# Performance work log

Measured on AMD Instinct MI355X. Metric: run time of the kernel, lower is better.

The kernel has to match this reference:

```python
import jax, jax.numpy as jnp
import numpy as np

B = 8192
W = 48            # target-net width
P = 4849          # flat param size of target MLP(1->48->48->48->1)
HW = 96           # hypernet width = 2*W
STEPS = 20
LR = 0.1
B1, B2, EPS = 0.9, 0.999, 1e-8


def setup_inputs() -> dict:
    key = jax.random.key(0)
    ks = jax.random.split(key, 6)
    x = jax.random.normal(ks[0], (B, 1), dtype=jnp.float32)
    c = jax.random.normal(ks[1], (B, 1), dtype=jnp.float32)
    # hypernet params (Linear(2,96) -> relu -> Linear(96,4849)), He-ish scaling
    hw1 = jax.random.normal(ks[2], (HW, 2), dtype=jnp.float32) / jnp.sqrt(2.0)
    hb1 = jax.random.normal(ks[3], (HW,), dtype=jnp.float32) * 0.1
    hw2 = jax.random.normal(ks[4], (P, HW), dtype=jnp.float32) / jnp.sqrt(float(HW))
    hb2 = jax.random.normal(ks[5], (P,), dtype=jnp.float32) * 0.1
    return {"x": x, "c": c, "hw1": hw1, "hb1": hb1, "hw2": hw2, "hb2": hb2}


def _target_apply(p, y):
    # unflatten per tree_flatten order: (w,b) per Linear layer of MLP(1,48,48,48,1)
    w0 = p[0:48].reshape(W, 1);      b0 = p[48:96]
    w1 = p[96:2400].reshape(W, W);   b1 = p[2400:2448]
    w2 = p[2448:4752].reshape(W, W); b2 = p[4752:4800]
    w3 = p[4800:4848].reshape(1, W); b3 = p[4848:4849]
    h = jax.nn.swish(w0 @ y + b0)
    h = jax.nn.swish(w1 @ h + b1)
    h = jax.nn.swish(w2 @ h + b2)
    return jnp.squeeze(w3 @ h + b3)


def _taylor_energy_y(energy_fn, y_target, y_anchor):
    # 2nd-order Taylor expansion via nested JVPs (order_y == 2)
    tangent = y_target - y_anchor

    def grad_energy(y):
        return jax.jvp(energy_fn, (y,), (tangent,))[1]

    e0, term1 = jax.jvp(energy_fn, (y_anchor,), (tangent,))
    _, term2 = jax.jvp(grad_energy, (y_anchor,), (tangent,))
    return e0 + term1 + 0.5 * term2


def _energy(y, p, y_anchor):
    return _taylor_energy_y(lambda yi: _target_apply(p, yi), y, y_anchor)


_grad_fn = jax.vmap(jax.grad(_energy), in_axes=(0, 0, 0))  # grad wrt y only


def reference(x, c, hw1, hb1, hw2, hb2):
    hyper_in = jnp.concatenate([x, c], axis=1)                 # (B, 2)
    h = jax.nn.relu(hyper_in @ hw1.T + hb1)                    # (B, 96)
    flat_params = h @ hw2.T + hb2                              # (B, P)

    y0 = jnp.zeros((x.shape[0], 1), dtype=x.dtype)             # y_mean = 0.0
    m0 = jnp.zeros_like(y0)
    v0 = jnp.zeros_like(y0)

    def step(carry, _):
        y, m, v, t = carry
        g = _grad_fn(y, flat_params, y)  # key=None -> anchor y0 = y_curr
        t = t + 1
        m = B1 * m + (1.0 - B1) * g
        v = B2 * v + (1.0 - B2) * g * g
        mh = m / (1.0 - jnp.power(B1, t))
        vh = v / (1.0 - jnp.power(B2, t))
        y = y - LR * mh / (jnp.sqrt(vh) + EPS)
        return (y, m, v, t), None

    (y_final, _, _, _), _ = jax.lax.scan(
        step, (y0, m0, v0, jnp.asarray(0, jnp.int32)), None, length=STEPS)
    return y_final
```

## Files before the change

kernel.cpp:

```cpp
#include <hip/hip_runtime.h>
#include <cstdint>
#include <cstddef>

#define NB    8192
#define NP    4849
#define NW    48
#define NCH   38
#define GY    64

typedef __attribute__((ext_vector_type(8))) _Float16 f16x8;
typedef __attribute__((ext_vector_type(4))) float f32x4;
typedef __attribute__((ext_vector_type(2))) float f32x2;

__device__ __forceinline__ const float* pptr(const float* Pp, int i, int rp) {
  return Pp + ((size_t)(rp >> 7) * NB + i) * 128 + (rp & 127);
}

__device__ __forceinline__ int invperm(int rp) {
  if (rp >= 96 && rp < 2400) {
    int t = rp - 96; int kb = t / 192; int rem = t - kb * 192;
    return 96 + (rem >> 2) * 48 + (kb * 4 + (rem & 3));
  }
  if (rp >= 2448 && rp < 4752) {
    int t = rp - 2448; int kb = t / 192; int rem = t - kb * 192;
    return 2448 + (rem >> 2) * 48 + (kb * 4 + (rem & 3));
  }
  return rp;
}

__global__ __launch_bounds__(256, 2) void hyper_gemm(
    const float* __restrict__ x, const float* __restrict__ c,
    const float* __restrict__ hw1, const float* __restrict__ hb1,
    const float* __restrict__ hw2, const float* __restrict__ hb2,
    float* __restrict__ Pp)
{
  const int t    = threadIdx.x;
  const int lane = t & 63;
  const int wv   = t >> 6;
  const int m16  = lane & 15;
  const int q    = lane >> 4;
  const int rp0  = blockIdx.x * 128;

  const float* wr[2];
  float bias[2];
  #pragma unroll
  for (int nt = 0; nt < 2; ++nt) {
    int rp = rp0 + wv * 32 + nt * 16 + m16;
    int r  = (rp < NP) ? invperm(rp) : 0;
    wr[nt]   = hw2 + (size_t)r * 96;
    bias[nt] = (rp < NP) ? hb2[r] : 0.f;
  }

  f16x8 bh[3][2], bl[3][2];
  #pragma unroll
  for (int ch = 0; ch < 3; ++ch) {
    const int k0 = ch * 32 + q * 8;
    #pragma unroll
    for (int nt = 0; nt < 2; ++nt) {
      float4 f0 = *(const float4*)(wr[nt] + k0);
      float4 f1 = *(const float4*)(wr[nt] + k0 + 4);
      float fv[8] = {f0.x,f0.y,f0.z,f0.w,f1.x,f1.y,f1.z,f1.w};
      #pragma unroll
      for (int e = 0; e < 8; ++e) {
        _Float16 hi = (_Float16)fv[e];
        float r = fv[e] - (float)hi;
        bh[ch][nt][e] = hi;
        bl[ch][nt][e] = (_Float16)r;
      }
    }
  }

  float* cbase = Pp + (size_t)blockIdx.x * NB * 128;

  for (int mtile = blockIdx.y; mtile < 128; mtile += GY) {
    const int i0 = mtile * 64;

    float xv[4], cv[4];
    #pragma unroll
    for (int mt = 0; mt < 4; ++mt) {
      int i = i0 + mt * 16 + m16;
      xv[mt] = x[i]; cv[mt] = c[i];
    }

    f32x4 acc[4][2];
    #pragma unroll
    for (int mt = 0; mt < 4; ++mt)
      #pragma unroll
      for (int nt = 0; nt < 2; ++nt)
        acc[mt][nt] = (f32x4){0.f, 0.f, 0.f, 0.f};

    #pragma unroll
    for (int ch = 0; ch < 3; ++ch) {
      const int k0 = ch * 32 + q * 8;

      float4 A0 = *(const float4*)(hw1 + 2 * k0);
      float4 A1 = *(const float4*)(hw1 + 2 * k0 + 4);
      float4 A2 = *(const float4*)(hw1 + 2 * k0 + 8);
      float4 A3 = *(const float4*)(hw1 + 2 * k0 + 12);
      float4 B0 = *(const float4*)(hb1 + k0);
      float4 B1 = *(const float4*)(hb1 + k0 + 4);
      float w0k[8] = {A0.x,A0.z,A1.x,A1.z,A2.x,A2.z,A3.x,A3.z};
      float w1k[8] = {A0.y,A0.w,A1.y,A1.w,A2.y,A2.w,A3.y,A3.w};
      float bk[8]  = {B0.x,B0.y,B0.z,B0.w,B1.x,B1.y,B1.z,B1.w};

      f16x8 ah[4], al[4];
      #pragma unroll
      for (int mt = 0; mt < 4; ++mt) {
        #pragma unroll
        for (int j = 0; j < 8; ++j) {
          float h = fmaf(xv[mt], w0k[j], fmaf(cv[mt], w1k[j], bk[j]));
          h = h > 0.f ? h : 0.f;
          _Float16 hi = (_Float16)h;
          float r = h - (float)hi;
          ah[mt][j] = hi;
          al[mt][j] = (_Float16)r;
        }
      }

      #pragma unroll
      for (int mt = 0; mt < 4; ++mt)
        #pragma unroll
        for (int nt = 0; nt < 2; ++nt) {
          acc[mt][nt] = __builtin_amdgcn_mfma_f32_16x16x32_f16(al[mt], bl[ch][nt], acc[mt][nt], 0, 0, 0);
          acc[mt][nt] = __builtin_amdgcn_mfma_f32_16x16x32_f16(ah[mt], bl[ch][nt], acc[mt][nt], 0, 0, 0);
          acc[mt][nt] = __builtin_amdgcn_mfma_f32_16x16x32_f16(al[mt], bh[ch][nt], acc[mt][nt], 0, 0, 0);
          acc[mt][nt] = __builtin_amdgcn_mfma_f32_16x16x32_f16(ah[mt], bh[ch][nt], acc[mt][nt], 0, 0, 0);
        }
    }

    #pragma unroll
    for (int nt = 0; nt < 2; ++nt) {
      int off = wv * 32 + nt * 16 + m16;
      if (rp0 + off < NP) {
        #pragma unroll
        for (int mt = 0; mt < 4; ++mt)
          #pragma unroll
          for (int r = 0; r < 4; ++r) {
            int i = i0 + mt * 16 + q * 4 + r;
            cbase[(size_t)i * 128 + off] = acc[mt][nt][r] + bias[nt];
          }
      }
    }
  }
}


#define DPP_ADD(x, ctrl, rmask)                                               \
  (x) += __int_as_float(__builtin_amdgcn_update_dpp(                          \
      0, __float_as_int(x), (ctrl), (rmask), 0xf, false))

__global__ __launch_bounds__(64, 2) void adam_inner(
    const float* __restrict__ Pp, float* __restrict__ out)
{
  __shared__ __align__(16) float hd[2][96];

  const int lane = threadIdx.x;
  const int i    = blockIdx.x;
  const bool act = lane < NW;

  float* buf0 = &hd[0][0];
  float* buf1 = &hd[1][0];

  float w0  = act ? *pptr(Pp, i, lane)        : 0.f;
  float b0  = act ? *pptr(Pp, i, 48 + lane)   : 0.f;
  float b1v = act ? *pptr(Pp, i, 2400 + lane) : 0.f;
  float b2v = act ? *pptr(Pp, i, 4752 + lane) : 0.f;
  float w3  = act ? *pptr(Pp, i, 4800 + lane) : 0.f;

  f32x2 w1p[24], w2p[24];
  #pragma unroll
  for (int kb = 0; kb < 12; ++kb) {
    float4 q1 = *(const float4*)pptr(Pp, i, 96 + kb * 192 + lane * 4);
    w1p[2 * kb]     = (f32x2){q1.x, q1.y};
    w1p[2 * kb + 1] = (f32x2){q1.z, q1.w};
    float4 q2 = *(const float4*)pptr(Pp, i, 2448 + kb * 192 + lane * 4);
    w2p[2 * kb]     = (f32x2){q2.x, q2.y};
    w2p[2 * kb + 1] = (f32x2){q2.z, q2.w};
  }

  float y = 0.f, m = 0.f, v = 0.f;
  float b1t = 1.f, b2t = 1.f;

  #pragma unroll 1
  for (int t = 0; t < 20; ++t) {
    float z  = fmaf(w0, y, b0);
    float s  = __builtin_amdgcn_rcpf(1.f + __expf(-z));
    float h  = z * s;
    float dh = fmaf(z * s, 1.f - s, s) * w0;
    if (act) { buf0[lane] = h; buf0[48 + lane] = dh; }

    float4 ph[12], pd[12];
    #pragma unroll
    for (int kk = 0; kk < 12; ++kk) {
      ph[kk] = *(const float4*)(buf0 + 4 * kk);
      pd[kk] = *(const float4*)(buf0 + 48 + 4 * kk);
    }
    {
      f32x2 zz[4] = {(f32x2){b1v, 0.f}, (f32x2){0.f, 0.f},
                     (f32x2){0.f, 0.f}, (f32x2){0.f, 0.f}};
      f32x2 dd[4] = {(f32x2){0.f, 0.f}, (f32x2){0.f, 0.f},
                     (f32x2){0.f, 0.f}, (f32x2){0.f, 0.f}};
      #pragma unroll
      for (int kk = 0; kk < 12; ++kk) {
        int c0 = (2 * kk) & 3, c1 = (2 * kk + 1) & 3;
        zz[c0] = __builtin_elementwise_fma(w1p[2 * kk],     (f32x2){ph[kk].x, ph[kk].y}, zz[c0]);
        zz[c1] = __builtin_elementwise_fma(w1p[2 * kk + 1], (f32x2){ph[kk].z, ph[kk].w}, zz[c1]);
        dd[c0] = __builtin_elementwise_fma(w1p[2 * kk],     (f32x2){pd[kk].x, pd[kk].y}, dd[c0]);
        dd[c1] = __builtin_elementwise_fma(w1p[2 * kk + 1], (f32x2){pd[kk].z, pd[kk].w}, dd[c1]);
      }
      f32x2 zs = (zz[0] + zz[1]) + (zz[2] + zz[3]);
      f32x2 ds = (dd[0] + dd[1]) + (dd[2] + dd[3]);
      float z1  = zs.x + zs.y;
      float dz1 = ds.x + ds.y;

      s  = __builtin_amdgcn_rcpf(1.f + __expf(-z1));
      h  = z1 * s;
      dh = fmaf(h, 1.f - s, s) * dz1;
    }
    if (act) { buf1[lane] = h; buf1[48 + lane] = dh; }

    #pragma unroll
    for (int kk = 0; kk < 12; ++kk) {
      ph[kk] = *(const float4*)(buf1 + 4 * kk);
      pd[kk] = *(const float4*)(buf1 + 48 + 4 * kk);
    }
    {
      f32x2 zz[4] = {(f32x2){b2v, 0.f}, (f32x2){0.f, 0.f},
                     (f32x2){0.f, 0.f}, (f32x2){0.f, 0.f}};
      f32x2 dd[4] = {(f32x2){0.f, 0.f}, (f32x2){0.f, 0.f},
                     (f32x2){0.f, 0.f}, (f32x2){0.f, 0.f}};
      #pragma unroll
      for (int kk = 0; kk < 12; ++kk) {
        int c0 = (2 * kk) & 3, c1 = (2 * kk + 1) & 3;
        zz[c0] = __builtin_elementwise_fma(w2p[2 * kk],     (f32x2){ph[kk].x, ph[kk].y}, zz[c0]);
        zz[c1] = __builtin_elementwise_fma(w2p[2 * kk + 1], (f32x2){ph[kk].z, ph[kk].w}, zz[c1]);
        dd[c0] = __builtin_elementwise_fma(w2p[2 * kk],     (f32x2){pd[kk].x, pd[kk].y}, dd[c0]);
        dd[c1] = __builtin_elementwise_fma(w2p[2 * kk + 1], (f32x2){pd[kk].z, pd[kk].w}, dd[c1]);
      }
      f32x2 zs = (zz[0] + zz[1]) + (zz[2] + zz[3]);
      f32x2 ds = (dd[0] + dd[1]) + (dd[2] + dd[3]);
      float z2  = zs.x + zs.y;
      float dz2 = ds.x + ds.y;

      s  = __builtin_amdgcn_rcpf(1.f + __expf(-z2));
      dh = fmaf(z2 * s, 1.f - s, s) * dz2;
    }

    float r = act ? w3 * dh : 0.f;
    DPP_ADD(r, 0x111, 0xf);
    DPP_ADD(r, 0x112, 0xf);
    DPP_ADD(r, 0x114, 0xf);
    DPP_ADD(r, 0x118, 0xf);
    DPP_ADD(r, 0x142, 0xa);
    DPP_ADD(r, 0x143, 0xc);
    float g = __int_as_float(__builtin_amdgcn_readlane(__float_as_int(r), 63));

    m = fmaf(0.9f,   m, 0.1f   * g);
    v = fmaf(0.999f, v, 0.001f * g * g);
    b1t *= 0.9f; b2t *= 0.999f;
    float mh  = m * __builtin_amdgcn_rcpf(1.f - b1t);
    float vh  = v * __builtin_amdgcn_rcpf(1.f - b2t);
    float den = __builtin_amdgcn_sqrtf(vh) + 1e-8f;
    y -= 0.1f * mh * __builtin_amdgcn_rcpf(den);
  }

  if (lane == 0) out[i] = y;
}

extern "C" void kernel_launch(void* const* d_in, const int* in_sizes, int n_in,
                              void* d_out, int out_size, void* d_ws, size_t ws_size,
                              hipStream_t stream) {
  const float* x   = (const float*)d_in[0];
  const float* c   = (const float*)d_in[1];
  const float* hw1 = (const float*)d_in[2];
  const float* hb1 = (const float*)d_in[3];
  const float* hw2 = (const float*)d_in[4];
  const float* hb2 = (const float*)d_in[5];
  float* Pp  = (float*)d_ws;
  float* out = (float*)d_out;

  dim3 gridB(NCH, GY);
  hyper_gemm<<<gridB, dim3(256), 0, stream>>>(x, c, hw1, hb1, hw2, hb2, Pp);
  adam_inner<<<dim3(8192), dim3(64), 0, stream>>>(Pp, out);
}
```

Baseline: 204.3 us.

## Pack two batch items per wavefront with 1.5 hidden units per lane

Each 64-lane wave now processes two batch items, with 32 lanes per item and each lane owning one unit plus, for the lower 16 lanes, a second unit. This halves the grid and amortizes per-wave LDS exchange and reduction overhead across two items. The half-wave reduction ends with a ds_bpermute instead of readlane. Register usage roughly doubles for weights, and the launch bound drops to one wave per SIMD hint, which risks lower occupancy and latency hiding.

```diff
diff --git a/kernel.cpp b/kernel.cpp
--- a/kernel.cpp
+++ b/kernel.cpp
@@ -149,111 +149,152 @@
   (x) += __int_as_float(__builtin_amdgcn_update_dpp(                          \
       0, __float_as_int(x), (ctrl), (rmask), 0xf, false))
 
-__global__ __launch_bounds__(64, 2) void adam_inner(
+__global__ __launch_bounds__(64, 1) void adam_inner(
     const float* __restrict__ Pp, float* __restrict__ out)
 {
-  __shared__ __align__(16) float hd[2][96];
+  __shared__ __align__(16) float hd[2][2][96];
 
   const int lane = threadIdx.x;
-  const int i    = blockIdx.x;
-  const bool act = lane < NW;
-
-  float* buf0 = &hd[0][0];
-  float* buf1 = &hd[1][0];
-
-  float w0  = act ? *pptr(Pp, i, lane)        : 0.f;
-  float b0  = act ? *pptr(Pp, i, 48 + lane)   : 0.f;
-  float b1v = act ? *pptr(Pp, i, 2400 + lane) : 0.f;
-  float b2v = act ? *pptr(Pp, i, 4752 + lane) : 0.f;
-  float w3  = act ? *pptr(Pp, i, 4800 + lane) : 0.f;
-
-  f32x2 w1p[24], w2p[24];
+  const int half = lane >> 5;
+  const int sl   = lane & 31;
+  const int item = blockIdx.x * 2 + half;
+  const bool act1 = sl < 16;
+
+  const int u0 = sl;
+  const int u1 = 32 + (sl & 15);
+
+  float* my0 = &hd[half][0][0];
+  float* my1 = &hd[half][1][0];
+
+  float w0a  = *pptr(Pp, item, u0);
+  float b0a  = *pptr(Pp, item, 48 + u0);
+  float b1va = *pptr(Pp, item, 2400 + u0);
+  float b2va = *pptr(Pp, item, 4752 + u0);
+  float w3a  = *pptr(Pp, item, 4800 + u0);
+  float w0b  = act1 ? *pptr(Pp, item, u1)        : 0.f;
+  float b0b  = act1 ? *pptr(Pp, item, 48 + u1)   : 0.f;
+  float b1vb = act1 ? *pptr(Pp, item, 2400 + u1) : 0.f;
+  float b2vb = act1 ? *pptr(Pp, item, 4752 + u1) : 0.f;
+  float w3b  = act1 ? *pptr(Pp, item, 4800 + u1) : 0.f;
+
+  f32x2 w1a[24], w2a[24], w1b[24], w2b[24];
   #pragma unroll
   for (int kb = 0; kb < 12; ++kb) {
-    float4 q1 = *(const float4*)pptr(Pp, i, 96 + kb * 192 + lane * 4);
-    w1p[2 * kb]     = (f32x2){q1.x, q1.y};
-    w1p[2 * kb + 1] = (f32x2){q1.z, q1.w};
-    float4 q2 = *(const float4*)pptr(Pp, i, 2448 + kb * 192 + lane * 4);
-    w2p[2 * kb]     = (f32x2){q2.x, q2.y};
-    w2p[2 * kb + 1] = (f32x2){q2.z, q2.w};
-  }
+    float4 q1 = *(const float4*)pptr(Pp, item, 96 + kb * 192 + u0 * 4);
+    w1a[2 * kb]     = (f32x2){q1.x, q1.y};
+    w1a[2 * kb + 1] = (f32x2){q1.z, q1.w};
+    float4 q2 = *(const float4*)pptr(Pp, item, 2448 + kb * 192 + u0 * 4);
+    w2a[2 * kb]     = (f32x2){q2.x, q2.y};
+    w2a[2 * kb + 1] = (f32x2){q2.z, q2.w};
+    float4 q3 = *(const float4*)pptr(Pp, item, 96 + kb * 192 + u1 * 4);
+    if (!act1) q3 = (float4){0.f, 0.f, 0.f, 0.f};
+    w1b[2 * kb]     = (f32x2){q3.x, q3.y};
+    w1b[2 * kb + 1] = (f32x2){q3.z, q3.w};
+    float4 q4 = *(const float4*)pptr(Pp, item, 2448 + kb * 192 + u1 * 4);
+    if (!act1) q4 = (float4){0.f, 0.f, 0.f, 0.f};
+    w2b[2 * kb]     = (f32x2){q4.x, q4.y};
+    w2b[2 * kb + 1] = (f32x2){q4.z, q4.w};
+  }
+
+  const int bidx = ((lane & 32) | 31) << 2;
 
   float y = 0.f, m = 0.f, v = 0.f;
   float b1t = 1.f, b2t = 1.f;
 
   #pragma unroll 1
   for (int t = 0; t < 20; ++t) {
-    float z  = fmaf(w0, y, b0);
-    float s  = __builtin_amdgcn_rcpf(1.f + __expf(-z));
-    float h  = z * s;
-    float dh = fmaf(z * s, 1.f - s, s) * w0;
-    if (act) { buf0[lane] = h; buf0[48 + lane] = dh; }
-
-    float4 ph[12], pd[12];
-    #pragma unroll
-    for (int kk = 0; kk < 12; ++kk) {
-      ph[kk] = *(const float4*)(buf0 + 4 * kk);
-      pd[kk] = *(const float4*)(buf0 + 48 + 4 * kk);
-    }
-    {
-      f32x2 zz[4] = {(f32x2){b1v, 0.f}, (f32x2){0.f, 0.f},
-                     (f32x2){0.f, 0.f}, (f32x2){0.f, 0.f}};
-      f32x2 dd[4] = {(f32x2){0.f, 0.f}, (f32x2){0.f, 0.f},
-                     (f32x2){0.f, 0.f}, (f32x2){0.f, 0.f}};
+    {
+      float z  = fmaf(w0a, y, b0a);
+      float s  = __builtin_amdgcn_rcpf(1.f + __expf(-z));
+      float h  = z * s;
+      float dh = fmaf(h, 1.f - s, s) * w0a;
+      my0[u0] = h; my0[48 + u0] = dh;
+      float zb  = fmaf(w0b, y, b0b);
+      float sb  = __builtin_amdgcn_rcpf(1.f + __expf(-zb));
+      float hb  = zb * sb;
+      float dhb = fmaf(hb, 1.f - sb, sb) * w0b;
+      if (act1) { my0[u1] = hb; my0[48 + u1] = dhb; }
+    }
+
+    float z1a, dz1a, z1b, dz1b;
+    {
+      f32x2 za[2] = {(f32x2){b1va, 0.f}, (f32x2){0.f, 0.f}};
+      f32x2 da[2] = {(f32x2){0.f, 0.f}, (f32x2){0.f, 0.f}};
+      f32x2 zb[2] = {(f32x2){b1vb, 0.f}, (f32x2){0.f, 0.f}};
+      f32x2 db[2] = {(f32x2){0.f, 0.f}, (f32x2){0.f, 0.f}};
       #pragma unroll
       for (int kk = 0; kk < 12; ++kk) {
-        int c0 = (2 * kk) & 3, c1 = (2 * kk + 1) & 3;
-        zz[c0] = __builtin_elementwise_fma(w1p[2 * kk],     (f32x2){ph[kk].x, ph[kk].y}, zz[c0]);
-        zz[c1] = __builtin_elementwise_fma(w1p[2 * kk + 1], (f32x2){ph[kk].z, ph[kk].w}, zz[c1]);
-        dd[c0] = __builtin_elementwise_fma(w1p[2 * kk],     (f32x2){pd[kk].x, pd[kk].y}, dd[c0]);
-        dd[c1] = __builtin_elementwise_fma(w1p[2 * kk + 1], (f32x2){pd[kk].z, pd[kk].w}, dd[c1]);
-      }
-      f32x2 zs = (zz[0] + zz[1]) + (zz[2] + zz[3]);
-      f32x2 ds = (dd[0] + dd[1]) + (dd[2] + dd[3]);
-      float z1  = zs.x + zs.y;
-      float dz1 = ds.x + ds.y;
-
-      s  = __builtin_amdgcn_rcpf(1.f + __expf(-z1));
-      h  = z1 * s;
-      dh = fmaf(h, 1.f - s, s) * dz1;
-    }
-    if (act) { buf1[lane] = h; buf1[48 + lane] = dh; }
-
-    #pragma unroll
-    for (int kk = 0; kk < 12; ++kk) {
-      ph[kk] = *(const float4*)(buf1 + 4 * kk);
-      pd[kk] = *(const float4*)(buf1 + 48 + 4 * kk);
-    }
-    {
-      f32x2 zz[4] = {(f32x2){b2v, 0.f}, (f32x2){0.f, 0.f},
-                     (f32x2){0.f, 0.f}, (f32x2){0.f, 0.f}};
-      f32x2 dd[4] = {(f32x2){0.f, 0.f}, (f32x2){0.f, 0.f},
-                     (f32x2){0.f, 0.f}, (f32x2){0.f, 0.f}};
+        float4 ph = *(const float4*)(my0 + 4 * kk);
+        float4 pd = *(const float4*)(my0 + 48 + 4 * kk);
+        int c = kk & 1;
+        za[c] = __builtin_elementwise_fma(w1a[2 * kk],     (f32x2){ph.x, ph.y}, za[c]);
+        za[c] = __builtin_elementwise_fma(w1a[2 * kk + 1], (f32x2){ph.z, ph.w}, za[c]);
+        da[c] = __builtin_elementwise_fma(w1a[2 * kk],     (f32x2){pd.x, pd.y}, da[c]);
+        da[c] = __builtin_elementwise_fma(w1a[2 * kk + 1], (f32x2){pd.z, pd.w}, da[c]);
+        zb[c] = __builtin_elementwise_fma(w1b[2 * kk],     (f32x2){ph.x, ph.y}, zb[c]);
+        zb[c] = __builtin_elementwise_fma(w1b[2 * kk + 1], (f32x2){ph.z, ph.w}, zb[c]);
+        db[c] = __builtin_elementwise_fma(w1b[2 * kk],     (f32x2){pd.x, pd.y}, db[c]);
+        db[c] = __builtin_elementwise_fma(w1b[2 * kk + 1], (f32x2){pd.z, pd.w}, db[c]);
+      }
+      f32x2 zsa = za[0] + za[1], dsa = da[0] + da[1];
+      f32x2 zsb = zb[0] + zb[1], dsb = db[0] + db[1];
+      z1a = zsa.x + zsa.y; dz1a = dsa.x + dsa.y;
+      z1b = zsb.x + zsb.y; dz1b = dsb.x + dsb.y;
+    }
+
+    {
+      float s  = __builtin_amdgcn_rcpf(1.f + __expf(-z1a));
+      float h  = z1a * s;
+      float dh = fmaf(h, 1.f - s, s) * dz1a;
+      my1[u0] = h; my1[48 + u0] = dh;
+      float sb  = __builtin_amdgcn_rcpf(1.f + __expf(-z1b));
+      float hb  = z1b * sb;
+      float dhb = fmaf(hb, 1.f - sb, sb) * dz1b;
+      if (act1) { my1[u1] = hb; my1[48 + u1] = dhb; }
+    }
+
+    float z2a, dz2a, z2b, dz2b;
+    {
+      f32x2 za[2] = {(f32x2){b2va, 0.f}, (f32x2){0.f, 0.f}};
+      f32x2 da[2] = {(f32x2){0.f, 0.f}, (f32x2){0.f, 0.f}};
+      f32x2 zb[2] = {(f32x2){b2vb, 0.f}, (f32x2){0.f, 0.f}};
+      f32x2 db[2] = {(f32x2){0.f, 0.f}, (f32x2){0.f, 0.f}};
       #pragma unroll
       for (int kk = 0; kk < 12; ++kk) {
-        int c0 = (2 * kk) & 3, c1 = (2 * kk + 1) & 3;
-        zz[c0] = __builtin_elementwise_fma(w2p[2 * kk],     (f32x2){ph[kk].x, ph[kk].y}, zz[c0]);
-        zz[c1] = __builtin_elementwise_fma(w2p[2 * kk + 1], (f32x2){ph[kk].z, ph[kk].w}, zz[c1]);
-        dd[c0] = __builtin_elementwise_fma(w2p[2 * kk],     (f32x2){pd[kk].x, pd[kk].y}, dd[c0]);
-        dd[c1] = __builtin_elementwise_fma(w2p[2 * kk + 1], (f32x2){pd[kk].z, pd[kk].w}, dd[c1]);
-      }
-      f32x2 zs = (zz[0] + zz[1]) + (zz[2] + zz[3]);
-      f32x2 ds = (dd[0] + dd[1]) + (dd[2] + dd[3]);
-      float z2  = zs.x + zs.y;
-      float dz2 = ds.x + ds.y;
-
-      s  = __builtin_amdgcn_rcpf(1.f + __expf(-z2));
-      dh = fmaf(z2 * s, 1.f - s, s) * dz2;
-    }
-
-    float r = act ? w3 * dh : 0.f;
-    DPP_ADD(r, 0x111, 0xf);
-    DPP_ADD(r, 0x112, 0xf);
-    DPP_ADD(r, 0x114, 0xf);
-    DPP_ADD(r, 0x118, 0xf);
-    DPP_ADD(r, 0x142, 0xa);
-    DPP_ADD(r, 0x143, 0xc);
-    float g = __int_as_float(__builtin_amdgcn_readlane(__float_as_int(r), 63));
+        float4 ph = *(const float4*)(my1 + 4 * kk);
+        float4 pd = *(const float4*)(my1 + 48 + 4 * kk);
+        int c = kk & 1;
+        za[c] = __builtin_elementwise_fma(w2a[2 * kk],     (f32x2){ph.x, ph.y}, za[c]);
+        za[c] = __builtin_elementwise_fma(w2a[2 * kk + 1], (f32x2){ph.z, ph.w}, za[c]);
+        da[c] = __builtin_elementwise_fma(w2a[2 * kk],     (f32x2){pd.x, pd.y}, da[c]);
+        da[c] = __builtin_elementwise_fma(w2a[2 * kk + 1], (f32x2){pd.z, pd.w}, da[c]);
+        zb[c] = __builtin_elementwise_fma(w2b[2 * kk],     (f32x2){ph.x, ph.y}, zb[c]);
+        zb[c] = __builtin_elementwise_fma(w2b[2 * kk + 1], (f32x2){ph.z, ph.w}, zb[c]);
+        db[c] = __builtin_elementwise_fma(w2b[2 * kk],     (f32x2){pd.x, pd.y}, db[c]);
+        db[c] = __builtin_elementwise_fma(w2b[2 * kk + 1], (f32x2){pd.z, pd.w}, db[c]);
+      }
+      f32x2 zsa = za[0] + za[1], dsa = da[0] + da[1];
+      f32x2 zsb = zb[0] + zb[1], dsb = db[0] + db[1];
+      z2a = zsa.x + zsa.y; dz2a = dsa.x + dsa.y;
+      z2b = zsb.x + zsb.y; dz2b = dsb.x + dsb.y;
+    }
+
+    float part;
+    {
+      float s  = __builtin_amdgcn_rcpf(1.f + __expf(-z2a));
+      float d3 = fmaf(z2a * s, 1.f - s, s) * dz2a;
+      part = w3a * d3;
+      float sb  = __builtin_amdgcn_rcpf(1.f + __expf(-z2b));
+      float d3b = fmaf(z2b * sb, 1.f - sb, sb) * dz2b;
+      part = fmaf(w3b, d3b, part);
+    }
+    DPP_ADD(part, 0x111, 0xf);
+    DPP_ADD(part, 0x112, 0xf);
+    DPP_ADD(part, 0x114, 0xf);
+    DPP_ADD(part, 0x118, 0xf);
+    DPP_ADD(part, 0x142, 0xa);
+    float g = __int_as_float(
+        __builtin_amdgcn_ds_bpermute(bidx, __float_as_int(part)));
 
     m = fmaf(0.9f,   m, 0.1f   * g);
     v = fmaf(0.999f, v, 0.001f * g * g);
@@ -264,7 +305,7 @@
     y -= 0.1f * mh * __builtin_amdgcn_rcpf(den);
   }
 
-  if (lane == 0) out[i] = y;
+  if (sl == 0) out[item] = y;
 }
 
 extern "C" void kernel_launch(void* const* d_in, const int* in_sizes, int n_in,
@@ -281,5 +322,5 @@
 
   dim3 gridB(NCH, GY);
   hyper_gemm<<<gridB, dim3(256), 0, stream>>>(x, c, hw1, hb1, hw2, hb2, Pp);
-  adam_inner<<<dim3(8192), dim3(64), 0, stream>>>(Pp, out);
-}
+  adam_inner<<<dim3(4096), dim3(64), 0, stream>>>(Pp, out);
+}
```

Result: slower. 252.4 us (+23.6%).
